# Optimization experiments

Hardware: AMD Instinct MI355X
Metric: run time of the kernel (lower is better)

The kernel has to match this reference:

```python
import jax, jax.numpy as jnp
import numpy as np

WORD_DICT_SIZE = 50002
POS_DICT_SIZE = 53
DEP_DICT_SIZE = 54
EMB = 128
UNITS = 100
B, T = 256, 256
IN_DIM = 3 * EMB  # 384


def setup_inputs() -> dict:
    key = jax.random.key(0)
    ks = jax.random.split(key, 12)
    words = jax.random.randint(ks[0], (B, T), 1, WORD_DICT_SIZE)
    pos = jax.random.randint(ks[1], (B, T), 1, POS_DICT_SIZE)
    dep = jax.random.randint(ks[2], (B, T), 1, DEP_DICT_SIZE)
    # ragged padding: index 0 is the mask token (mask_zero=True)
    lengths = jax.random.randint(ks[3], (B,), T // 2, T + 1)
    pad = jnp.arange(T)[None, :] >= lengths[:, None]
    words = jnp.where(pad, 0, words)
    pos = jnp.where(pad, 0, pos)
    dep = jnp.where(pad, 0, dep)

    def glorot(k, shape):
        lim = np.sqrt(6.0 / (shape[0] + shape[1]))
        return jax.random.uniform(k, shape, jnp.float32, -lim, lim)

    E_word = glorot(ks[4], (WORD_DICT_SIZE, EMB))
    E_pos = glorot(ks[5], (POS_DICT_SIZE, EMB))
    E_dep = glorot(ks[6], (DEP_DICT_SIZE, EMB))
    W_fwd = glorot(ks[7], (IN_DIM, 4 * UNITS))
    U_fwd = glorot(ks[8], (UNITS, 4 * UNITS))
    W_bwd = glorot(ks[9], (IN_DIM, 4 * UNITS))
    U_bwd = glorot(ks[10], (UNITS, 4 * UNITS))
    # Keras unit_forget_bias=True: forget-gate bias initialized to 1
    b = jnp.zeros((4 * UNITS,), jnp.float32).at[UNITS:2 * UNITS].set(1.0)
    W_out = glorot(ks[11], (2 * UNITS, 1))
    b_out = jnp.zeros((1,), jnp.float32)
    return {"words": words, "pos": pos, "dep": dep,
            "E_word": E_word, "E_pos": E_pos, "E_dep": E_dep,
            "W_fwd": W_fwd, "U_fwd": U_fwd, "b_fwd": b,
            "W_bwd": W_bwd, "U_bwd": U_bwd, "b_bwd": b,
            "W_out": W_out, "b_out": b_out}


def _masked_lstm(x_tbd, mask_tb, W, U, b, reverse):
    """Keras-style masked LSTM. x_tbd: [T,B,D], mask_tb: [T,B].
    Masked steps carry state/output through unchanged (zero_output_for_mask=False)."""
    units = U.shape[0]
    xw = jnp.einsum('tbd,dh->tbh', x_tbd, W) + b  # precompute input projection

    def step(carry, inp):
        h, c = carry
        xw_t, m = inp
        z = xw_t + h @ U
        i, f, g, o = jnp.split(z, 4, axis=-1)
        i = jax.nn.sigmoid(i)
        f = jax.nn.sigmoid(f)
        g = jnp.tanh(g)
        o = jax.nn.sigmoid(o)
        c_new = f * c + i * g
        h_new = o * jnp.tanh(c_new)
        m = m[:, None]
        h2 = jnp.where(m, h_new, h)
        c2 = jnp.where(m, c_new, c)
        return (h2, c2), h2

    h0 = jnp.zeros((x_tbd.shape[1], units), x_tbd.dtype)
    _, hs = jax.lax.scan(step, (h0, h0), (xw, mask_tb), reverse=reverse)
    return hs  # [T,B,units]


def reference(words, pos, dep, E_word, E_pos, E_dep,
              W_fwd, U_fwd, b_fwd, W_bwd, U_bwd, b_bwd, W_out, b_out):
    mask = words != 0  # [B,T]
    x = jnp.concatenate([E_word[words], E_pos[pos], E_dep[dep]], axis=-1)  # [B,T,384]
    xt = jnp.transpose(x, (1, 0, 2))  # [T,B,384]
    mt = mask.T                        # [T,B]
    h_f = _masked_lstm(xt, mt, W_fwd, U_fwd, b_fwd, reverse=False)
    h_b = _masked_lstm(xt, mt, W_bwd, U_bwd, b_bwd, reverse=True)
    h = jnp.concatenate([h_f, h_b], axis=-1)          # [T,B,200]
    h = jnp.transpose(h, (1, 0, 2))                    # [B,T,200]
    out = jax.nn.sigmoid(h @ W_out + b_out)[..., 0]    # [B,T]
    return out
```

## Files before the change

kernel.cpp:

```cpp
#include <hip/hip_runtime.h>
#include <hip/hip_bf16.h>

#define T_LEN 256
#define B_SZ  256
#define EMB   128
#define UNITS 100
#define GATES 400
#define NCOL  800
#define NQ    52

typedef __attribute__((ext_vector_type(8))) short short8v;
typedef __attribute__((ext_vector_type(4))) short short4v;
typedef __attribute__((ext_vector_type(4))) float f32x4;
typedef _Float16 half2v __attribute__((ext_vector_type(2)));

static __device__ __forceinline__ float bf2f(short s) {
    unsigned u = ((unsigned)(unsigned short)s) << 16;
    return __builtin_bit_cast(float, u);
}
static __device__ __forceinline__ short f2bf(float f) {
    return __builtin_bit_cast(short, __float2bfloat16(f));
}
static __device__ __forceinline__ float fast_sigmoid(float x) {
    return 1.f / (1.f + __expf(-x));
}
static __device__ __forceinline__ float fast_tanh(float x) {
    return 1.f - 2.f / (1.f + __expf(2.f * x));
}
static __device__ __forceinline__ float fdot2p(unsigned hp, unsigned up, float c) {
#if __has_builtin(__builtin_amdgcn_fdot2)
    return __builtin_amdgcn_fdot2(__builtin_bit_cast(half2v, hp),
                                  __builtin_bit_cast(half2v, up), c, false);
#else
    const half2v a = __builtin_bit_cast(half2v, hp);
    const half2v b = __builtin_bit_cast(half2v, up);
    return fmaf((float)a[1], (float)b[1], fmaf((float)a[0], (float)b[0], c));
#endif
}

#define PREP_WT_BLOCKS 100
#define PREP_TAB_BLOCKS 107
#define PREP_UPK_BLOCKS 21

__global__ __launch_bounds__(256) void prep(
    const float* __restrict__ Wf, const float* __restrict__ Wb,
    const float* __restrict__ bf_, const float* __restrict__ bb_,
    const float* __restrict__ Ep, const float* __restrict__ Ed,
    const float* __restrict__ Uf, const float* __restrict__ Ub,
    __hip_bfloat16* __restrict__ WbT, float* __restrict__ Ppos,
    float* __restrict__ Pdep, unsigned* __restrict__ Upk, int* __restrict__ flag)
{
    __shared__ short Ap[16 * 32];
    __shared__ short Bp[32 * 16];

    const int bx = blockIdx.x, tid = threadIdx.x;

    if (bx < PREP_WT_BLOCKS) {
        const int base = bx * 1024 + tid * 4;
#pragma unroll
        for (int q = 0; q < 4; ++q) {
            const int id = base + q;
            const int c = id >> 7, k = id & 127;
            const int dir = c >= GATES;
            const int j = c - dir * GATES;
            const float* W = dir ? Wb : Wf;
            WbT[id] = __float2bfloat16(W[k * GATES + j]);
        }
    } else if (bx < PREP_WT_BLOCKS + PREP_TAB_BLOCKS) {
        const int p = bx - PREP_WT_BLOCKS;
        const bool isPos = p < 53;
        const float* Erow = isPos ? (Ep + p * EMB) : (Ed + (size_t)(p - 53) * EMB);
        const int rowoff = isPos ? EMB : 2 * EMB;
        float* dst = isPos ? (Ppos + (size_t)p * NCOL) : (Pdep + (size_t)(p - 53) * NCOL);
        for (int c = tid; c < NCOL; c += 256) {
            const int dir = c >= GATES;
            const int j = c - dir * GATES;
            const float* W = dir ? Wb : Wf;
            float s = 0.f;
            for (int k = 0; k < EMB; ++k)
                s = fmaf(Erow[k], W[(size_t)(rowoff + k) * GATES + j], s);
            if (!isPos) s += (dir ? bb_[j] : bf_[j]);
            dst[c] = s;
        }
    } else if (bx < PREP_WT_BLOCKS + PREP_TAB_BLOCKS + PREP_UPK_BLOCKS) {
        const int p2 = bx - PREP_WT_BLOCKS - PREP_TAB_BLOCKS;
#pragma unroll
        for (int i = 0; i < 8; ++i) {
            const int e = p2 * 2048 + tid * 8 + i;
            if (e < 2 * NQ * GATES) {
                const int dir = e / (NQ * GATES);
                const int rem = e - dir * (NQ * GATES);
                const int q = rem / GATES, jp = rem - q * GATES;
                const int unit = jp >> 2, gate = jp & 3;
                const int jorig = gate * UNITS + unit;
                const float* U = dir ? Ub : Uf;
                const int k0 = 2 * q, k1 = 2 * q + 1;
                const float v0 = (k0 < UNITS) ? U[(size_t)k0 * GATES + jorig] : 0.f;
                const float v1 = (k1 < UNITS) ? U[(size_t)k1 * GATES + jorig] : 0.f;
                const unsigned lo = (unsigned)(unsigned short)__builtin_bit_cast(short, (_Float16)v0);
                const unsigned hi = (unsigned)(unsigned short)__builtin_bit_cast(short, (_Float16)v1);
                Upk[e] = lo | (hi << 16);
            }
        }
    } else {
        if (tid < 64) {
            for (int e = tid; e < 512; e += 64) {
                const int m = e >> 5, k = e & 31;
                Ap[e] = f2bf((float)((m * 3 + k * 5) % 7 - 3));
            }
            for (int e = tid; e < 512; e += 64) {
                const int k = e >> 4, n = e & 15;
                Bp[e] = f2bf((float)((k * 7 + n * 3) % 5 - 2));
            }
        }
        __syncthreads();
        if (tid < 64) {
            const int l = tid, mn = l & 15, grp = l >> 4;
            float ref[4];
#pragma unroll
            for (int i = 0; i < 4; ++i) {
                const int m = grp * 4 + i;
                float s = 0.f;
                for (int k = 0; k < 32; ++k)
                    s += bf2f(Ap[m * 32 + k]) * bf2f(Bp[k * 16 + mn]);
                ref[i] = s;
            }
            short8v a8, b8;
#pragma unroll
            for (int e = 0; e < 8; ++e) {
                const int k8 = grp * 8 + e;
                a8[e] = Ap[mn * 32 + k8];
                b8[e] = Bp[k8 * 16 + mn];
            }
            f32x4 z = {0.f, 0.f, 0.f, 0.f};
            f32x4 d8 = __builtin_amdgcn_mfma_f32_16x16x32_bf16(a8, b8, z, 0, 0, 0);
            const bool ok8 = (d8[0] == ref[0]) && (d8[1] == ref[1]) &&
                             (d8[2] == ref[2]) && (d8[3] == ref[3]);
            const unsigned long long m8 = __ballot(ok8);
            if (tid == 0) flag[0] = (m8 == ~0ULL) ? 0 : 1;
        }
    }
}

#define MT 64
#define NT 160

__global__ __launch_bounds__(256) void embed_gemm(
    const int* __restrict__ words, const int* __restrict__ pos, const int* __restrict__ dep,
    const float* __restrict__ Ew, const __hip_bfloat16* __restrict__ WbT,
    const float* __restrict__ Ppos, const float* __restrict__ Pdep,
    const int* __restrict__ flag, __hip_bfloat16* __restrict__ xw)
{
    __shared__ __align__(16) short As[MT * 128];
    __shared__ __align__(16) short Bs[NT * 128];
    __shared__ int widx[MT], pidx[MT], didx[MT];

    const int tid = threadIdx.x;
    const int bx = blockIdx.x, by = blockIdx.y;
    const int r0 = bx * MT;
    const int t = r0 >> 8, b0 = r0 & 255;
    const int n0 = by * NT;

    if (tid < MT)             widx[tid]          = words[(size_t)(b0 + tid) * T_LEN + t];
    else if (tid < 2 * MT)    pidx[tid - MT]     = pos[(size_t)(b0 + tid - MT) * T_LEN + t];
    else if (tid < 3 * MT)    didx[tid - 2 * MT] = dep[(size_t)(b0 + tid - 2 * MT) * T_LEN + t];
    __syncthreads();

#pragma unroll
    for (int q = 0; q < 4; ++q) {
        const int ch = tid + q * 256;
        const int row = ch >> 4, c16 = ch & 15;
        const float* src = Ew + (size_t)widx[row] * EMB + c16 * 8;
        const float4 v0 = *reinterpret_cast<const float4*>(src);
        const float4 v1 = *reinterpret_cast<const float4*>(src + 4);
        short8v pk;
        pk[0] = f2bf(v0.x); pk[1] = f2bf(v0.y); pk[2] = f2bf(v0.z); pk[3] = f2bf(v0.w);
        pk[4] = f2bf(v1.x); pk[5] = f2bf(v1.y); pk[6] = f2bf(v1.z); pk[7] = f2bf(v1.w);
        *reinterpret_cast<short8v*>(&As[row * 128 + ((c16 ^ (row & 7)) << 3)]) = pk;
    }
#pragma unroll
    for (int q = 0; q < 10; ++q) {
        const int ch = tid + q * 256;
        const int col = ch >> 4, c16 = ch & 15;
        const short* src = reinterpret_cast<const short*>(WbT) + (size_t)(n0 + col) * 128 + c16 * 8;
        const short8v v = *reinterpret_cast<const short8v*>(src);
        *reinterpret_cast<short8v*>(&Bs[col * 128 + ((c16 ^ (col & 7)) << 3)]) = v;
    }
    __syncthreads();

    const int w = tid >> 6, l = tid & 63;
    const int lr = l & 15, lg = l >> 4;
    const int arow = w * 16 + lr;

    f32x4 acc[10];
#pragma unroll
    for (int ni = 0; ni < 10; ++ni) acc[ni] = f32x4{0.f, 0.f, 0.f, 0.f};

    const int lay = flag[0];

    if (lay == 0) {
#pragma unroll
        for (int kk = 0; kk < 4; ++kk) {
            const int c16 = kk * 4 + lg;
            const short8v a = *reinterpret_cast<const short8v*>(
                &As[arow * 128 + ((c16 ^ (arow & 7)) << 3)]);
#pragma unroll
            for (int ni = 0; ni < 10; ++ni) {
                const int col = ni * 16 + lr;
                const short8v bfr = *reinterpret_cast<const short8v*>(
                    &Bs[col * 128 + ((c16 ^ (col & 7)) << 3)]);
                acc[ni] = __builtin_amdgcn_mfma_f32_16x16x32_bf16(a, bfr, acc[ni], 0, 0, 0);
            }
        }
    } else {
#pragma unroll
        for (int kk = 0; kk < 4; ++kk) {
            const int ch16 = kk * 4 + (lg >> 1);
            const int inner = (lg & 1) * 4;
            const int alo_i = arow * 128 + ((ch16 ^ (arow & 7)) << 3) + inner;
            const int ahi_i = arow * 128 + (((ch16 + 2) ^ (arow & 7)) << 3) + inner;
            const short4v alo = *reinterpret_cast<const short4v*>(&As[alo_i]);
            const short4v ahi = *reinterpret_cast<const short4v*>(&As[ahi_i]);
            short8v a;
            a[0] = alo[0]; a[1] = alo[1]; a[2] = alo[2]; a[3] = alo[3];
            a[4] = ahi[0]; a[5] = ahi[1]; a[6] = ahi[2]; a[7] = ahi[3];
#pragma unroll
            for (int ni = 0; ni < 10; ++ni) {
                const int col = ni * 16 + lr;
                const int blo_i = col * 128 + ((ch16 ^ (col & 7)) << 3) + inner;
                const int bhi_i = col * 128 + (((ch16 + 2) ^ (col & 7)) << 3) + inner;
                const short4v blo = *reinterpret_cast<const short4v*>(&Bs[blo_i]);
                const short4v bhi = *reinterpret_cast<const short4v*>(&Bs[bhi_i]);
                short8v b;
                b[0] = blo[0]; b[1] = blo[1]; b[2] = blo[2]; b[3] = blo[3];
                b[4] = bhi[0]; b[5] = bhi[1]; b[6] = bhi[2]; b[7] = bhi[3];
                acc[ni] = __builtin_amdgcn_mfma_f32_16x16x32_bf16(a, b, acc[ni], 0, 0, 0);
            }
        }
    }

    const int rbase = w * 16 + lg * 4;
    int pix[4], dix[4];
#pragma unroll
    for (int i = 0; i < 4; ++i) { pix[i] = pidx[rbase + i]; dix[i] = didx[rbase + i]; }
#pragma unroll
    for (int ni = 0; ni < 10; ++ni) {
        const int c = n0 + ni * 16 + lr;
        const int dirg = c >= GATES;
        const int j = c - dirg * GATES;
        const int gate = j / UNITS, unit = j - gate * UNITS;
        const int cperm = dirg * GATES + unit * 4 + gate;
#pragma unroll
        for (int i = 0; i < 4; ++i) {
            const float v = acc[ni][i]
                          + Ppos[(size_t)pix[i] * NCOL + c]
                          + Pdep[(size_t)dix[i] * NCOL + c];
            xw[(size_t)(r0 + rbase + i) * NCOL + cperm] = __float2bfloat16(v);
        }
    }
}

#define BAR() do { \
    asm volatile("s_waitcnt lgkmcnt(0)" ::: "memory"); \
    __builtin_amdgcn_sched_barrier(0); \
    __builtin_amdgcn_s_barrier(); \
    __builtin_amdgcn_sched_barrier(0); \
} while (0)

__global__ __launch_bounds__(448, 1) void lstm_valu(
    const int* __restrict__ words,
    const __hip_bfloat16* __restrict__ xw,
    const unsigned* __restrict__ Upk,
    _Float16* __restrict__ h_f, _Float16* __restrict__ h_b)
{
    const int b = blockIdx.x >> 1, dirv = blockIdx.x & 1;
    _Float16* hout = dirv ? h_b : h_f;
    const int coff = dirv * GATES;
    const unsigned* up = Upk + (size_t)dirv * NQ * GATES;

    __shared__ __align__(16) _Float16 h_buf[2][104];
    __shared__ unsigned char m_sh[T_LEN];

    const int tid = threadIdx.x;
    const bool isCol = tid < GATES;
    const int colid = isCol ? tid : (GATES - 1);
    const int unit = colid >> 2, gate = colid & 3;

    for (int i = tid; i < T_LEN; i += 448)
        m_sh[i] = (unsigned char)(words[(size_t)b * T_LEN + i] != 0);
    if (tid < 104) reinterpret_cast<unsigned*>(&h_buf[0][0])[tid] = 0u;

    unsigned upk[NQ];
#pragma unroll
    for (int q = 0; q < NQ; ++q) upk[q] = up[q * GATES + colid];
#pragma unroll
    for (int q = 0; q < NQ; ++q) asm volatile("" : "+v"(upk[q]));

    float c = 0.f, h = 0.f;
    __syncthreads();

    const int t0 = dirv ? (T_LEN - 1) : 0;
    const int dt = dirv ? -1 : 1;
    const short* xs = reinterpret_cast<const short*>(xw);

    short pf = 0;
    if (isCol) pf = xs[((size_t)t0 * B_SZ + b) * NCOL + coff + colid];

    int p = 0;
    for (int s = 0; s < T_LEN; ++s) {
        const int t = t0 + dt * s;
        int tn = t + dt; tn = tn < 0 ? 0 : (tn > T_LEN - 1 ? T_LEN - 1 : tn);

        short pfn = pf;
        if (isCol) {
            const float zx = bf2f(pf);
            pfn = xs[((size_t)tn * B_SZ + b) * NCOL + coff + colid];
            float a0 = 0.f, a1 = 0.f, a2 = 0.f, a3 = 0.f;
            const uint4* h4 = reinterpret_cast<const uint4*>(&h_buf[p][0]);
#pragma unroll
            for (int qq = 0; qq < 13; ++qq) {
                const uint4 hv = h4[qq];
                a0 = fdot2p(hv.x, upk[4 * qq + 0], a0);
                a1 = fdot2p(hv.y, upk[4 * qq + 1], a1);
                a2 = fdot2p(hv.z, upk[4 * qq + 2], a2);
                a3 = fdot2p(hv.w, upk[4 * qq + 3], a3);
            }
            const float z = zx + (a0 + a1) + (a2 + a3);
            const float zz  = (gate == 2) ? 2.f * z : z;
            const float sg  = fast_sigmoid(zz);
            const float act = (gate == 2) ? (2.f * sg - 1.f) : sg;
            const float v1 = __shfl_xor(act, 1);
            const float v2 = __shfl_xor(act, 2);
            const float v3 = __shfl_xor(act, 3);
            if (gate == 0) {
                const float cn = v1 * c + act * v2;
                const float hn = v3 * fast_tanh(cn);
                const bool m = m_sh[t] != 0;
                h = m ? hn : h;
                c = m ? cn : c;
                const _Float16 hh = (_Float16)h;
                h_buf[p ^ 1][unit] = hh;
                hout[((size_t)t * B_SZ + b) * UNITS + unit] = hh;
            }
        }
        pf = pfn;

        BAR();
        p ^= 1;
    }
}

__global__ __launch_bounds__(256) void out_proj(
    const _Float16* __restrict__ h_f, const _Float16* __restrict__ h_b,
    const float* __restrict__ Wo, const float* __restrict__ bo,
    float* __restrict__ out)
{
    const int tid = threadIdx.x;
    const int g = tid >> 2, sub = tid & 3;
    const int r = blockIdx.x * 64 + g;
    const int t = r >> 8, b = r & 255;

    const _Float16* hf = h_f + (size_t)r * UNITS;
    const _Float16* hb = h_b + (size_t)r * UNITS;

    float s = 0.f;
    const int k0 = sub * 25;
#pragma unroll
    for (int k = 0; k < 25; ++k) s = fmaf((float)hf[k0 + k], Wo[k0 + k], s);
#pragma unroll
    for (int k = 0; k < 25; ++k) s = fmaf((float)hb[k0 + k], Wo[UNITS + k0 + k], s);

    s += __shfl_xor(s, 1);
    s += __shfl_xor(s, 2);

    if (sub == 0)
        out[(size_t)b * T_LEN + t] = 1.f / (1.f + __expf(-(s + bo[0])));
}

extern "C" void kernel_launch(void* const* d_in, const int* in_sizes, int n_in,
                              void* d_out, int out_size, void* d_ws, size_t ws_size,
                              hipStream_t stream)
{
    const int*   words = (const int*)d_in[0];
    const int*   pos   = (const int*)d_in[1];
    const int*   dep   = (const int*)d_in[2];
    const float* Ew    = (const float*)d_in[3];
    const float* Ep    = (const float*)d_in[4];
    const float* Ed    = (const float*)d_in[5];
    const float* Wf    = (const float*)d_in[6];
    const float* Uf    = (const float*)d_in[7];
    const float* bf_   = (const float*)d_in[8];
    const float* Wb    = (const float*)d_in[9];
    const float* Ub    = (const float*)d_in[10];
    const float* bb_   = (const float*)d_in[11];
    const float* Wo    = (const float*)d_in[12];
    const float* bo    = (const float*)d_in[13];
    float* out = (float*)d_out;

    auto alignup = [](size_t x) { return (x + 255) & ~(size_t)255; };
    char* p = (char*)d_ws;
    __hip_bfloat16* xw = (__hip_bfloat16*)p;  p += alignup((size_t)T_LEN * B_SZ * NCOL * 2);
    _Float16* h_f = (_Float16*)p;             p += alignup((size_t)T_LEN * B_SZ * UNITS * 2);
    _Float16* h_b = (_Float16*)p;             p += alignup((size_t)T_LEN * B_SZ * UNITS * 2);
    __hip_bfloat16* WbT = (__hip_bfloat16*)p; p += alignup((size_t)NCOL * 128 * 2);
    float* Ppos = (float*)p;                  p += alignup((size_t)53 * NCOL * 4);
    float* Pdep = (float*)p;                  p += alignup((size_t)54 * NCOL * 4);
    unsigned* Upk = (unsigned*)p;             p += alignup((size_t)2 * NQ * GATES * 4);
    int* flag = (int*)p;

    prep<<<dim3(PREP_WT_BLOCKS + PREP_TAB_BLOCKS + PREP_UPK_BLOCKS + 1), 256, 0, stream>>>(
        Wf, Wb, bf_, bb_, Ep, Ed, Uf, Ub, WbT, Ppos, Pdep, Upk, flag);

    embed_gemm<<<dim3((T_LEN * B_SZ) / MT, NCOL / NT), 256, 0, stream>>>(
        words, pos, dep, Ew, WbT, Ppos, Pdep, flag, xw);

    lstm_valu<<<dim3(B_SZ * 2), 448, 0, stream>>>(words, xw, Upk, h_f, h_b);

    out_proj<<<dim3((T_LEN * B_SZ) / 64), 256, 0, stream>>>(h_f, h_b, Wo, bo, out);
}
```

Measured before the change: 403.1 us.

## Split LSTM recurrent dot product across two threads per gate column

Each gate column of the recurrent matvec is now handled by two threads, each covering half of the hidden vector, and the partial sums are combined with a lane shuffle. The block grows from 448 to 832 threads, and the per-thread packed U registers drop from 52 to 28. This shortens the serial per-step dependency chain. The xw output is no longer permuted in the GEMM epilogue; the LSTM instead reads the original column layout directly. The cost is more waves per barrier, an extra shuffle, and uncoalesced xw loads.

```diff
diff --git a/kernel.cpp b/kernel.cpp
--- a/kernel.cpp
+++ b/kernel.cpp
@@ -7,7 +7,8 @@
 #define UNITS 100
 #define GATES 400
 #define NCOL  800
-#define NQ    52
+#define NPAIR 56
+#define NP    28
 
 typedef __attribute__((ext_vector_type(8))) short short8v;
 typedef __attribute__((ext_vector_type(4))) short short4v;
@@ -40,7 +41,7 @@
 
 #define PREP_WT_BLOCKS 100
 #define PREP_TAB_BLOCKS 107
-#define PREP_UPK_BLOCKS 21
+#define PREP_UPK_BLOCKS 22
 
 __global__ __launch_bounds__(256) void prep(
     const float* __restrict__ Wf, const float* __restrict__ Wb,
@@ -87,14 +88,14 @@
 #pragma unroll
         for (int i = 0; i < 8; ++i) {
             const int e = p2 * 2048 + tid * 8 + i;
-            if (e < 2 * NQ * GATES) {
-                const int dir = e / (NQ * GATES);
-                const int rem = e - dir * (NQ * GATES);
-                const int q = rem / GATES, jp = rem - q * GATES;
+            if (e < 2 * NPAIR * GATES) {
+                const int dir = e / (NPAIR * GATES);
+                const int rem = e - dir * (NPAIR * GATES);
+                const int pp = rem / GATES, jp = rem - pp * GATES;
                 const int unit = jp >> 2, gate = jp & 3;
                 const int jorig = gate * UNITS + unit;
                 const float* U = dir ? Ub : Uf;
-                const int k0 = 2 * q, k1 = 2 * q + 1;
+                const int k0 = 2 * pp, k1 = 2 * pp + 1;
                 const float v0 = (k0 < UNITS) ? U[(size_t)k0 * GATES + jorig] : 0.f;
                 const float v1 = (k1 < UNITS) ? U[(size_t)k1 * GATES + jorig] : 0.f;
                 const unsigned lo = (unsigned)(unsigned short)__builtin_bit_cast(short, (_Float16)v0);
@@ -246,16 +247,12 @@
 #pragma unroll
     for (int ni = 0; ni < 10; ++ni) {
         const int c = n0 + ni * 16 + lr;
-        const int dirg = c >= GATES;
-        const int j = c - dirg * GATES;
-        const int gate = j / UNITS, unit = j - gate * UNITS;
-        const int cperm = dirg * GATES + unit * 4 + gate;
 #pragma unroll
         for (int i = 0; i < 4; ++i) {
             const float v = acc[ni][i]
                           + Ppos[(size_t)pix[i] * NCOL + c]
                           + Pdep[(size_t)dix[i] * NCOL + c];
-            xw[(size_t)(r0 + rbase + i) * NCOL + cperm] = __float2bfloat16(v);
+            xw[(size_t)(r0 + rbase + i) * NCOL + c] = __float2bfloat16(v);
         }
     }
 }
@@ -267,7 +264,7 @@
     __builtin_amdgcn_sched_barrier(0); \
 } while (0)
 
-__global__ __launch_bounds__(448, 1) void lstm_valu(
+__global__ __launch_bounds__(832, 1) void lstm_valu(
     const int* __restrict__ words,
     const __hip_bfloat16* __restrict__ xw,
     const unsigned* __restrict__ Upk,
@@ -276,25 +273,28 @@
     const int b = blockIdx.x >> 1, dirv = blockIdx.x & 1;
     _Float16* hout = dirv ? h_b : h_f;
     const int coff = dirv * GATES;
-    const unsigned* up = Upk + (size_t)dirv * NQ * GATES;
-
-    __shared__ __align__(16) _Float16 h_buf[2][104];
+    const unsigned* up = Upk + (size_t)dirv * NPAIR * GATES;
+
+    __shared__ __align__(16) _Float16 h_buf[2][112];
     __shared__ unsigned char m_sh[T_LEN];
 
     const int tid = threadIdx.x;
-    const bool isCol = tid < GATES;
-    const int colid = isCol ? tid : (GATES - 1);
+    const int col = tid >> 1, half = tid & 1;
+    const bool act_col = col < GATES;
+    const int colid = act_col ? col : (GATES - 1);
     const int unit = colid >> 2, gate = colid & 3;
-
-    for (int i = tid; i < T_LEN; i += 448)
+    const int jorig = gate * UNITS + unit;
+    const bool leader = act_col && ((tid & 7) == 0);
+
+    for (int i = tid; i < T_LEN; i += 832)
         m_sh[i] = (unsigned char)(words[(size_t)b * T_LEN + i] != 0);
-    if (tid < 104) reinterpret_cast<unsigned*>(&h_buf[0][0])[tid] = 0u;
-
-    unsigned upk[NQ];
-#pragma unroll
-    for (int q = 0; q < NQ; ++q) upk[q] = up[q * GATES + colid];
-#pragma unroll
-    for (int q = 0; q < NQ; ++q) asm volatile("" : "+v"(upk[q]));
+    if (tid < 112) reinterpret_cast<unsigned*>(&h_buf[0][0])[tid] = 0u;
+
+    unsigned upk[NP];
+#pragma unroll
+    for (int q = 0; q < NP; ++q) upk[q] = up[(half * NP + q) * GATES + colid];
+#pragma unroll
+    for (int q = 0; q < NP; ++q) asm volatile("" : "+v"(upk[q]));
 
     float c = 0.f, h = 0.f;
     __syncthreads();
@@ -303,47 +303,45 @@
     const int dt = dirv ? -1 : 1;
     const short* xs = reinterpret_cast<const short*>(xw);
 
-    short pf = 0;
-    if (isCol) pf = xs[((size_t)t0 * B_SZ + b) * NCOL + coff + colid];
+    short pf = xs[((size_t)t0 * B_SZ + b) * NCOL + coff + jorig];
 
     int p = 0;
     for (int s = 0; s < T_LEN; ++s) {
         const int t = t0 + dt * s;
         int tn = t + dt; tn = tn < 0 ? 0 : (tn > T_LEN - 1 ? T_LEN - 1 : tn);
 
-        short pfn = pf;
-        if (isCol) {
-            const float zx = bf2f(pf);
-            pfn = xs[((size_t)tn * B_SZ + b) * NCOL + coff + colid];
-            float a0 = 0.f, a1 = 0.f, a2 = 0.f, a3 = 0.f;
-            const uint4* h4 = reinterpret_cast<const uint4*>(&h_buf[p][0]);
-#pragma unroll
-            for (int qq = 0; qq < 13; ++qq) {
-                const uint4 hv = h4[qq];
-                a0 = fdot2p(hv.x, upk[4 * qq + 0], a0);
-                a1 = fdot2p(hv.y, upk[4 * qq + 1], a1);
-                a2 = fdot2p(hv.z, upk[4 * qq + 2], a2);
-                a3 = fdot2p(hv.w, upk[4 * qq + 3], a3);
-            }
-            const float z = zx + (a0 + a1) + (a2 + a3);
-            const float zz  = (gate == 2) ? 2.f * z : z;
-            const float sg  = fast_sigmoid(zz);
-            const float act = (gate == 2) ? (2.f * sg - 1.f) : sg;
-            const float v1 = __shfl_xor(act, 1);
-            const float v2 = __shfl_xor(act, 2);
-            const float v3 = __shfl_xor(act, 3);
-            if (gate == 0) {
-                const float cn = v1 * c + act * v2;
-                const float hn = v3 * fast_tanh(cn);
-                const bool m = m_sh[t] != 0;
-                h = m ? hn : h;
-                c = m ? cn : c;
-                const _Float16 hh = (_Float16)h;
-                h_buf[p ^ 1][unit] = hh;
-                hout[((size_t)t * B_SZ + b) * UNITS + unit] = hh;
-            }
-        }
-        pf = pfn;
+        const float zx = bf2f(pf);
+        pf = xs[((size_t)tn * B_SZ + b) * NCOL + coff + jorig];
+
+        float a0 = 0.f, a1 = 0.f, a2 = 0.f, a3 = 0.f;
+        const uint4* h4 = reinterpret_cast<const uint4*>(&h_buf[p][0]) + half * 7;
+#pragma unroll
+        for (int qq = 0; qq < 7; ++qq) {
+            const uint4 hv = h4[qq];
+            a0 = fdot2p(hv.x, upk[4 * qq + 0], a0);
+            a1 = fdot2p(hv.y, upk[4 * qq + 1], a1);
+            a2 = fdot2p(hv.z, upk[4 * qq + 2], a2);
+            a3 = fdot2p(hv.w, upk[4 * qq + 3], a3);
+        }
+        const float zpart = (a0 + a1) + (a2 + a3);
+        const float z = zx + zpart + __shfl_xor(zpart, 1);
+
+        const float zz  = (gate == 2) ? 2.f * z : z;
+        const float sg  = fast_sigmoid(zz);
+        const float act = (gate == 2) ? (2.f * sg - 1.f) : sg;
+        const float v1 = __shfl_xor(act, 2);
+        const float v2 = __shfl_xor(act, 4);
+        const float v3 = __shfl_xor(act, 6);
+        if (leader) {
+            const float cn = v1 * c + act * v2;
+            const float hn = v3 * fast_tanh(cn);
+            const bool m = m_sh[t] != 0;
+            h = m ? hn : h;
+            c = m ? cn : c;
+            const _Float16 hh = (_Float16)h;
+            h_buf[p ^ 1][unit] = hh;
+            hout[((size_t)t * B_SZ + b) * UNITS + unit] = hh;
+        }
 
         BAR();
         p ^= 1;
@@ -405,7 +403,7 @@
     __hip_bfloat16* WbT = (__hip_bfloat16*)p; p += alignup((size_t)NCOL * 128 * 2);
     float* Ppos = (float*)p;                  p += alignup((size_t)53 * NCOL * 4);
     float* Pdep = (float*)p;                  p += alignup((size_t)54 * NCOL * 4);
-    unsigned* Upk = (unsigned*)p;             p += alignup((size_t)2 * NQ * GATES * 4);
+    unsigned* Upk = (unsigned*)p;             p += alignup((size_t)2 * NPAIR * GATES * 4);
     int* flag = (int*)p;
 
     prep<<<dim3(PREP_WT_BLOCKS + PREP_TAB_BLOCKS + PREP_UPK_BLOCKS + 1), 256, 0, stream>>>(
@@ -414,7 +412,7 @@
     embed_gemm<<<dim3((T_LEN * B_SZ) / MT, NCOL / NT), 256, 0, stream>>>(
         words, pos, dep, Ew, WbT, Ppos, Pdep, flag, xw);
 
-    lstm_valu<<<dim3(B_SZ * 2), 448, 0, stream>>>(words, xw, Upk, h_f, h_b);
+    lstm_valu<<<dim3(B_SZ * 2), 832, 0, stream>>>(words, xw, Upk, h_f, h_b);
 
     out_proj<<<dim3((T_LEN * B_SZ) / 64), 256, 0, stream>>>(h_f, h_b, Wo, bo, out);
 }
```

Result: slower. 424.1 us (+5.2%).

## Broadcast hidden state via readlane and drop xw column permutation

Applied to the files above, without the earlier changes.

In the recurrent LSTM kernel, each wave now loads the 13 uint4 chunks of h into its first 13 lanes and broadcasts them with readlane, instead of every lane reading the whole h vector from LDS. The xw producer now writes columns in their original gate-major order, and the consumer indexes with gate*UNITS+unit, which removes the permutation arithmetic. The aim is to cut LDS traffic and latency on the serial per-step critical path, at the cost of 52 scalar readlanes per step and uncoalesced xw reads in the consumer.

```diff
diff --git a/kernel.cpp b/kernel.cpp
--- a/kernel.cpp
+++ b/kernel.cpp
@@ -246,16 +246,12 @@
 #pragma unroll
     for (int ni = 0; ni < 10; ++ni) {
         const int c = n0 + ni * 16 + lr;
-        const int dirg = c >= GATES;
-        const int j = c - dirg * GATES;
-        const int gate = j / UNITS, unit = j - gate * UNITS;
-        const int cperm = dirg * GATES + unit * 4 + gate;
 #pragma unroll
         for (int i = 0; i < 4; ++i) {
             const float v = acc[ni][i]
                           + Ppos[(size_t)pix[i] * NCOL + c]
                           + Pdep[(size_t)dix[i] * NCOL + c];
-            xw[(size_t)(r0 + rbase + i) * NCOL + cperm] = __float2bfloat16(v);
+            xw[(size_t)(r0 + rbase + i) * NCOL + c] = __float2bfloat16(v);
         }
     }
 }
@@ -282,9 +278,12 @@
     __shared__ unsigned char m_sh[T_LEN];
 
     const int tid = threadIdx.x;
-    const bool isCol = tid < GATES;
-    const int colid = isCol ? tid : (GATES - 1);
+    const int lane = tid & 63;
+    const bool act_col = tid < GATES;
+    const int colid = act_col ? tid : (GATES - 1);
     const int unit = colid >> 2, gate = colid & 3;
+    const int jorig = gate * UNITS + unit;
+    const bool leader = act_col && (gate == 0);
 
     for (int i = tid; i < T_LEN; i += 448)
         m_sh[i] = (unsigned char)(words[(size_t)b * T_LEN + i] != 0);
@@ -303,47 +302,50 @@
     const int dt = dirv ? -1 : 1;
     const short* xs = reinterpret_cast<const short*>(xw);
 
-    short pf = 0;
-    if (isCol) pf = xs[((size_t)t0 * B_SZ + b) * NCOL + coff + colid];
+    short pf = xs[((size_t)t0 * B_SZ + b) * NCOL + coff + jorig];
 
     int p = 0;
     for (int s = 0; s < T_LEN; ++s) {
         const int t = t0 + dt * s;
         int tn = t + dt; tn = tn < 0 ? 0 : (tn > T_LEN - 1 ? T_LEN - 1 : tn);
 
-        short pfn = pf;
-        if (isCol) {
-            const float zx = bf2f(pf);
-            pfn = xs[((size_t)tn * B_SZ + b) * NCOL + coff + colid];
-            float a0 = 0.f, a1 = 0.f, a2 = 0.f, a3 = 0.f;
-            const uint4* h4 = reinterpret_cast<const uint4*>(&h_buf[p][0]);
-#pragma unroll
-            for (int qq = 0; qq < 13; ++qq) {
-                const uint4 hv = h4[qq];
-                a0 = fdot2p(hv.x, upk[4 * qq + 0], a0);
-                a1 = fdot2p(hv.y, upk[4 * qq + 1], a1);
-                a2 = fdot2p(hv.z, upk[4 * qq + 2], a2);
-                a3 = fdot2p(hv.w, upk[4 * qq + 3], a3);
-            }
-            const float z = zx + (a0 + a1) + (a2 + a3);
-            const float zz  = (gate == 2) ? 2.f * z : z;
-            const float sg  = fast_sigmoid(zz);
-            const float act = (gate == 2) ? (2.f * sg - 1.f) : sg;
-            const float v1 = __shfl_xor(act, 1);
-            const float v2 = __shfl_xor(act, 2);
-            const float v3 = __shfl_xor(act, 3);
-            if (gate == 0) {
-                const float cn = v1 * c + act * v2;
-                const float hn = v3 * fast_tanh(cn);
-                const bool m = m_sh[t] != 0;
-                h = m ? hn : h;
-                c = m ? cn : c;
-                const _Float16 hh = (_Float16)h;
-                h_buf[p ^ 1][unit] = hh;
-                hout[((size_t)t * B_SZ + b) * UNITS + unit] = hh;
-            }
-        }
-        pf = pfn;
+        const float zx = bf2f(pf);
+        pf = xs[((size_t)tn * B_SZ + b) * NCOL + coff + jorig];
+
+        uint4 hv = {0u, 0u, 0u, 0u};
+        const uint4* h4 = reinterpret_cast<const uint4*>(&h_buf[p][0]);
+        if (lane < 13) hv = h4[lane];
+
+        float a0 = 0.f, a1 = 0.f, a2 = 0.f, a3 = 0.f;
+#pragma unroll
+        for (int qq = 0; qq < 13; ++qq) {
+            const unsigned h0 = (unsigned)__builtin_amdgcn_readlane((int)hv.x, qq);
+            const unsigned h1 = (unsigned)__builtin_amdgcn_readlane((int)hv.y, qq);
+            const unsigned h2 = (unsigned)__builtin_amdgcn_readlane((int)hv.z, qq);
+            const unsigned h3 = (unsigned)__builtin_amdgcn_readlane((int)hv.w, qq);
+            a0 = fdot2p(h0, upk[4 * qq + 0], a0);
+            a1 = fdot2p(h1, upk[4 * qq + 1], a1);
+            a2 = fdot2p(h2, upk[4 * qq + 2], a2);
+            a3 = fdot2p(h3, upk[4 * qq + 3], a3);
+        }
+        const float z = zx + (a0 + a1) + (a2 + a3);
+
+        const float zz  = (gate == 2) ? 2.f * z : z;
+        const float sg  = fast_sigmoid(zz);
+        const float act = (gate == 2) ? (2.f * sg - 1.f) : sg;
+        const float v1 = __shfl_xor(act, 1);
+        const float v2 = __shfl_xor(act, 2);
+        const float v3 = __shfl_xor(act, 3);
+        if (leader) {
+            const float cn = v1 * c + act * v2;
+            const float hn = v3 * fast_tanh(cn);
+            const bool m = m_sh[t] != 0;
+            h = m ? hn : h;
+            c = m ? cn : c;
+            const _Float16 hh = (_Float16)h;
+            h_buf[p ^ 1][unit] = hh;
+            hout[((size_t)t * B_SZ + b) * UNITS + unit] = hh;
+        }
 
         BAR();
         p ^= 1;
```

After: 434.2 us. 7.7% more time.
